# Performance work log

Measured on AMD Instinct MI355X. Metric: run time of the kernel, lower is better.

Reference implementation:

```python
import jax, jax.numpy as jnp
import numpy as np

N_NODES = 100000
N_EDGES = 1600000
IN_DIM = 128
OUT_DIM = 64


def setup_inputs() -> dict:
    key = jax.random.key(0)
    k1, k2, k3 = jax.random.split(key, 3)
    x = jax.random.normal(k1, (N_NODES, IN_DIM), dtype=jnp.float32)
    edge_index = jax.random.randint(k2, (2, N_EDGES), 0, N_NODES, dtype=jnp.int64)
    W = jax.random.normal(k3, (IN_DIM, OUT_DIM), dtype=jnp.float32) * (1.0 / np.sqrt(IN_DIM))
    b = jnp.zeros((OUT_DIM,), dtype=jnp.float32)
    return {"x": x, "edge_index": edge_index, "W": W, "b": b}


def reference(x, edge_index, W, b):
    row = edge_index[0]  # source nodes
    col = edge_index[1]  # target nodes (aggregation index)
    n = x.shape[0]

    # gcn_norm with add_self_loops=False: degree from edge weights (ones) at target
    ones = jnp.ones((edge_index.shape[1],), dtype=x.dtype)
    deg = jax.ops.segment_sum(ones, col, num_segments=n)  # [N]
    deg_inv_sqrt = jnp.where(deg > 0, jax.lax.rsqrt(jnp.maximum(deg, 1e-12)), 0.0)
    norm = deg_inv_sqrt[row] * deg_inv_sqrt[col]  # [E]

    # linear transform first (bias added after aggregation, as in PyG GCNConv)
    h = x @ W  # [N, OUT_DIM]

    # gather source features, scale by norm, scatter-add to targets
    msg = h[row] * norm[:, None]  # [E, OUT_DIM]
    out = jax.ops.segment_sum(msg, col, num_segments=n) + b  # [N, OUT_DIM]

    return jax.nn.relu(out)
```

## Files before the change

### kernel.cpp

```cpp
#include <hip/hip_runtime.h>
#include <hip/hip_bf16.h>

#define IN_DIM 128
#define OUT_DIM 64
#define FLOG 7
#define FNPB (1 << FLOG)
#define MAXFINE 1024
#define BB 512
#define BT 512
#define MAXE 8
#define NGRP 8
#define CAP_G 512
#define CAP (NGRP * CAP_G)
#define SPILL_MAX 65536

static inline size_t align_up(size_t v, size_t a) { return (v + a - 1) & ~(a - 1); }

__device__ __forceinline__ unsigned short f2bf(float f) {
    unsigned int x = __float_as_uint(f);
    unsigned int r = (x + 0x7fffu + ((x >> 16) & 1u)) >> 16;
    return (unsigned short)r;
}

typedef _Float16 half8 __attribute__((ext_vector_type(8)));
typedef float f32x4 __attribute__((ext_vector_type(4)));

__global__ void __launch_bounds__(BT, 4) k_build_mm(
    const int* __restrict__ row, const int* __restrict__ col,
    int* __restrict__ BinSize, unsigned int* __restrict__ EdgeBuf,
    uint2* __restrict__ spill, int* __restrict__ spillcur,
    const float* __restrict__ x, const float* __restrict__ W,
    unsigned short* __restrict__ h,
    int n_edges, int n_nodes, int nbf, int chunk, int mm_blocks) {
    if ((int)blockIdx.x < BB) {
        __shared__ int hist[MAXFINE];
        int t = threadIdx.x;
        int g = blockIdx.x & (NGRP - 1);
        int start = blockIdx.x * chunk;
        int end = min(n_edges, start + chunk);
        int n = end - start;

        for (int i = t; i < nbf; i += BT) hist[i] = 0;
        __syncthreads();

        int er[MAXE], ec[MAXE];
#pragma unroll
        for (int u = 0; u < MAXE; ++u) {
            int i = t + u * BT;
            ec[u] = -1;
            if (i < n) {
                er[u] = row[start + i];
                int c = col[start + i];
                ec[u] = c;
                atomicAdd(&hist[c >> FLOG], 1);
            }
        }
        __syncthreads();
        for (int i = t; i < nbf; i += BT) {
            int cv = hist[i];
            hist[i] = cv ? atomicAdd(&BinSize[g * nbf + i], cv) : 0;
        }
        __syncthreads();
#pragma unroll
        for (int u = 0; u < MAXE; ++u) {
            int c = ec[u];
            if (c >= 0) {
                int bin = c >> FLOG;
                int pos = atomicAdd(&hist[bin], 1);
                if (pos < CAP_G) {
                    EdgeBuf[(size_t)bin * CAP + g * CAP_G + pos] =
                        ((unsigned int)er[u] << FLOG) | (unsigned int)(c & (FNPB - 1));
                } else {
                    int sp = atomicAdd(spillcur, 1);
                    if (sp < SPILL_MAX)
                        spill[sp] = make_uint2((unsigned int)er[u], (unsigned int)c);
                }
            }
        }
    } else {
        const int lane = threadIdx.x & 63;
        const int m = lane & 15;
        const int q = lane >> 4;
        const int wv = threadIdx.x >> 6;
        const int wid0 = ((int)blockIdx.x - BB) * 8 + wv;
        const int nwaves = mm_blocks * 8;
        const int ntiles = (n_nodes + 15) >> 4;

        half8 bfrag[4][4];
#pragma unroll
        for (int kt = 0; kt < 4; ++kt) {
#pragma unroll
            for (int nt = 0; nt < 4; ++nt) {
                int k0 = kt * 32 + q * 8;
                int c = nt * 16 + m;
#pragma unroll
                for (int j = 0; j < 8; ++j)
                    bfrag[kt][nt][j] = (_Float16)W[(size_t)(k0 + j) * OUT_DIM + c];
            }
        }

        for (int wid = wid0; wid < ntiles; wid += nwaves) {
            const int nb = wid << 4;
            int arow = nb + m;
            if (arow >= n_nodes) arow = n_nodes - 1;
            const float* xr = x + (size_t)arow * IN_DIM;

            f32x4 acc[4];
#pragma unroll
            for (int nt = 0; nt < 4; ++nt) acc[nt] = (f32x4){0.f, 0.f, 0.f, 0.f};

#pragma unroll
            for (int kt = 0; kt < 4; ++kt) {
                const float4* xp = (const float4*)(xr + kt * 32 + q * 8);
                float4 lo = xp[0];
                float4 hi = xp[1];
                half8 afrag;
                afrag[0] = (_Float16)lo.x; afrag[1] = (_Float16)lo.y;
                afrag[2] = (_Float16)lo.z; afrag[3] = (_Float16)lo.w;
                afrag[4] = (_Float16)hi.x; afrag[5] = (_Float16)hi.y;
                afrag[6] = (_Float16)hi.z; afrag[7] = (_Float16)hi.w;
#pragma unroll
                for (int nt = 0; nt < 4; ++nt)
                    acc[nt] = __builtin_amdgcn_mfma_f32_16x16x32_f16(
                        afrag, bfrag[kt][nt], acc[nt], 0, 0, 0);
            }

#pragma unroll
            for (int r = 0; r < 4; ++r) {
                int node = nb + q * 4 + r;
                if (node < n_nodes) {
                    unsigned short* hp = h + (size_t)node * OUT_DIM + m;
#pragma unroll
                    for (int nt = 0; nt < 4; ++nt)
                        hp[nt * 16] = f2bf(acc[nt][r]);
                }
            }
        }
    }
}

__global__ void __launch_bounds__(256) kD_degree(
    const unsigned int* __restrict__ EdgeBuf, const int* __restrict__ BinSize,
    const uint2* __restrict__ spill, const int* __restrict__ spillcur,
    float* __restrict__ dis, int* __restrict__ cntg, int n_nodes, int nbf) {
    __shared__ int cnt[FNPB];
    int t = threadIdx.x;
    int b = blockIdx.x;
    if (t < FNPB) cnt[t] = 0;
    __syncthreads();
    for (int g = 0; g < NGRP; ++g) {
        int szg = min(BinSize[g * nbf + b], CAP_G);
        const unsigned int* sl = EdgeBuf + (size_t)b * CAP + g * CAP_G;
        for (int i = t; i < szg; i += 256)
            atomicAdd(&cnt[sl[i] & (FNPB - 1)], 1);
    }
    int sn = min(*spillcur, SPILL_MAX);
    for (int i = t; i < sn; i += 256) {
        uint2 e = spill[i];
        if ((int)(e.y >> FLOG) == b) atomicAdd(&cnt[e.y & (FNPB - 1)], 1);
    }
    __syncthreads();
    if (t < FNPB) {
        int d = cnt[t];
        cntg[(size_t)b * FNPB + t] = d;
        int node = (b << FLOG) + t;
        if (node < n_nodes)
            dis[node] = (d > 0) ? rsqrtf((float)d) : 0.0f;
    }
}

__global__ void __launch_bounds__(512) kF_sortagg(
    const unsigned int* __restrict__ EdgeBuf, const int* __restrict__ BinSize,
    const uint2* __restrict__ spill, const int* __restrict__ spillcur,
    const unsigned short* __restrict__ h, const float* __restrict__ dis,
    const int* __restrict__ cntg, const float* __restrict__ b,
    float* __restrict__ out, int* __restrict__ arena, int* __restrict__ arenacur,
    int n_nodes, int nbf) {
    __shared__ int cnt[FNPB];
    __shared__ int seg[FNPB];
    __shared__ int cursor[FNPB];
    __shared__ int sbuf[CAP];
    __shared__ int abase_sh;
    int t = threadIdx.x;
    int bk = blockIdx.x;
    int nb0 = bk << FLOG;
    int sn = min(*spillcur, SPILL_MAX);

    if (t < 64) {
        int2 cc = *(const int2*)(cntg + (size_t)bk * FNPB + 2 * t);
        int s = cc.x + cc.y;
#pragma unroll
        for (int off = 1; off < 64; off <<= 1) {
            int y = __shfl_up(s, off, 64);
            if (t >= off) s += y;
        }
        cnt[2 * t] = cc.x;
        cnt[2 * t + 1] = cc.y;
        seg[2 * t + 1] = s;
        seg[2 * t] = s - cc.y;
        cursor[2 * t] = s - cc.y - cc.x;
        cursor[2 * t + 1] = s - cc.y;
    }
    __syncthreads();

    int ne = seg[FNPB - 1];
    if (t == 0 && ne > CAP) abase_sh = atomicAdd(arenacur, ne);
    __syncthreads();

    const int lane = t & 63;
    const int wv = t >> 6;
    const int quarter = lane >> 4;
    const int qlane = lane & 15;
    float4 bias = ((const float4*)b)[qlane];

    if (ne <= CAP) {
        for (int g = 0; g < NGRP; ++g) {
            int szg = min(BinSize[g * nbf + bk], CAP_G);
            const unsigned int* sl = EdgeBuf + (size_t)bk * CAP + g * CAP_G;
            for (int i = t; i < szg; i += 512) {
                unsigned int v = sl[i];
                int p = atomicAdd(&cursor[v & (FNPB - 1)], 1);
                sbuf[p] = (int)(v >> FLOG);
            }
        }
        for (int i = t; i < sn; i += 512) {
            uint2 e = spill[i];
            if ((int)(e.y >> FLOG) == bk) {
                int p = atomicAdd(&cursor[e.y & (FNPB - 1)], 1);
                sbuf[p] = (int)e.x;
            }
        }
        __syncthreads();

        for (int nl = wv; nl < FNPB; nl += 8) {
            int node = nb0 + nl;
            if (node >= n_nodes) break;
            int e_ = seg[nl];
            int dcount = cnt[nl];
            int s_ = e_ - dcount;
            float a0 = 0.f, a1 = 0.f, a2 = 0.f, a3 = 0.f;
            for (int j0 = s_; j0 < e_; j0 += 16) {
                int i0 = j0 + quarter;
                int i1 = i0 + 4;
                int i2 = i0 + 8;
                int i3 = i0 + 12;
                int r0 = sbuf[i0 < e_ ? i0 : s_];
                int r1 = sbuf[i1 < e_ ? i1 : s_];
                int r2 = sbuf[i2 < e_ ? i2 : s_];
                int r3 = sbuf[i3 < e_ ? i3 : s_];
                float d0 = dis[r0];
                float d1 = dis[r1];
                float d2 = dis[r2];
                float d3 = dis[r3];
                uint2 v0 = make_uint2(0u, 0u), v1 = v0, v2 = v0, v3 = v0;
                if (i0 < e_)
                    v0 = *(const uint2*)(h + (size_t)r0 * OUT_DIM + qlane * 4);
                if (i1 < e_)
                    v1 = *(const uint2*)(h + (size_t)r1 * OUT_DIM + qlane * 4);
                if (i2 < e_)
                    v2 = *(const uint2*)(h + (size_t)r2 * OUT_DIM + qlane * 4);
                if (i3 < e_)
                    v3 = *(const uint2*)(h + (size_t)r3 * OUT_DIM + qlane * 4);
                a0 = fmaf(__uint_as_float(v0.x << 16), d0, a0);
                a1 = fmaf(__uint_as_float(v0.x & 0xFFFF0000u), d0, a1);
                a2 = fmaf(__uint_as_float(v0.y << 16), d0, a2);
                a3 = fmaf(__uint_as_float(v0.y & 0xFFFF0000u), d0, a3);
                a0 = fmaf(__uint_as_float(v1.x << 16), d1, a0);
                a1 = fmaf(__uint_as_float(v1.x & 0xFFFF0000u), d1, a1);
                a2 = fmaf(__uint_as_float(v1.y << 16), d1, a2);
                a3 = fmaf(__uint_as_float(v1.y & 0xFFFF0000u), d1, a3);
                a0 = fmaf(__uint_as_float(v2.x << 16), d2, a0);
                a1 = fmaf(__uint_as_float(v2.x & 0xFFFF0000u), d2, a1);
                a2 = fmaf(__uint_as_float(v2.y << 16), d2, a2);
                a3 = fmaf(__uint_as_float(v2.y & 0xFFFF0000u), d2, a3);
                a0 = fmaf(__uint_as_float(v3.x << 16), d3, a0);
                a1 = fmaf(__uint_as_float(v3.x & 0xFFFF0000u), d3, a1);
                a2 = fmaf(__uint_as_float(v3.y << 16), d3, a2);
                a3 = fmaf(__uint_as_float(v3.y & 0xFFFF0000u), d3, a3);
            }
            a0 += __shfl_xor(a0, 16, 64); a0 += __shfl_xor(a0, 32, 64);
            a1 += __shfl_xor(a1, 16, 64); a1 += __shfl_xor(a1, 32, 64);
            a2 += __shfl_xor(a2, 16, 64); a2 += __shfl_xor(a2, 32, 64);
            a3 += __shfl_xor(a3, 16, 64); a3 += __shfl_xor(a3, 32, 64);
            if (quarter == 0) {
                float dv = (dcount > 0) ? rsqrtf((float)dcount) : 0.0f;
                float4 o;
                o.x = fmaxf(fmaf(a0, dv, bias.x), 0.f);
                o.y = fmaxf(fmaf(a1, dv, bias.y), 0.f);
                o.z = fmaxf(fmaf(a2, dv, bias.z), 0.f);
                o.w = fmaxf(fmaf(a3, dv, bias.w), 0.f);
                ((float4*)(out + (size_t)node * OUT_DIM))[qlane] = o;
            }
        }
    } else {
        int abase = abase_sh;
        for (int g = 0; g < NGRP; ++g) {
            int szg = min(BinSize[g * nbf + bk], CAP_G);
            const unsigned int* sl = EdgeBuf + (size_t)bk * CAP + g * CAP_G;
            for (int i = t; i < szg; i += 512) {
                unsigned int v = sl[i];
                int p = atomicAdd(&cursor[v & (FNPB - 1)], 1);
                arena[abase + p] = (int)(v >> FLOG);
            }
        }
        for (int i = t; i < sn; i += 512) {
            uint2 e = spill[i];
            if ((int)(e.y >> FLOG) == bk) {
                int p = atomicAdd(&cursor[e.y & (FNPB - 1)], 1);
                arena[abase + p] = (int)e.x;
            }
        }
        __threadfence();
        __syncthreads();
        for (int nl = wv; nl < FNPB; nl += 8) {
            int node = nb0 + nl;
            if (node >= n_nodes) break;
            int e_ = seg[nl];
            int dcount = cnt[nl];
            int s_ = e_ - dcount;
            float a0 = 0.f, a1 = 0.f, a2 = 0.f, a3 = 0.f;
            for (int j0 = s_; j0 < e_; j0 += 8) {
                int iA = j0 + quarter;
                int iB = j0 + quarter + 4;
                int rA = arena[abase + (iA < e_ ? iA : s_)];
                int rB = arena[abase + (iB < e_ ? iB : s_)];
                float dA = dis[rA];
                float dB = dis[rB];
                uint2 vA = make_uint2(0u, 0u), vB = make_uint2(0u, 0u);
                if (iA < e_)
                    vA = *(const uint2*)(h + (size_t)rA * OUT_DIM + qlane * 4);
                if (iB < e_)
                    vB = *(const uint2*)(h + (size_t)rB * OUT_DIM + qlane * 4);
                a0 = fmaf(__uint_as_float(vA.x << 16), dA, a0);
                a1 = fmaf(__uint_as_float(vA.x & 0xFFFF0000u), dA, a1);
                a2 = fmaf(__uint_as_float(vA.y << 16), dA, a2);
                a3 = fmaf(__uint_as_float(vA.y & 0xFFFF0000u), dA, a3);
                a0 = fmaf(__uint_as_float(vB.x << 16), dB, a0);
                a1 = fmaf(__uint_as_float(vB.x & 0xFFFF0000u), dB, a1);
                a2 = fmaf(__uint_as_float(vB.y << 16), dB, a2);
                a3 = fmaf(__uint_as_float(vB.y & 0xFFFF0000u), dB, a3);
            }
            a0 += __shfl_xor(a0, 16, 64); a0 += __shfl_xor(a0, 32, 64);
            a1 += __shfl_xor(a1, 16, 64); a1 += __shfl_xor(a1, 32, 64);
            a2 += __shfl_xor(a2, 16, 64); a2 += __shfl_xor(a2, 32, 64);
            a3 += __shfl_xor(a3, 16, 64); a3 += __shfl_xor(a3, 32, 64);
            if (quarter == 0) {
                float dv = (dcount > 0) ? rsqrtf((float)dcount) : 0.0f;
                float4 o;
                o.x = fmaxf(fmaf(a0, dv, bias.x), 0.f);
                o.y = fmaxf(fmaf(a1, dv, bias.y), 0.f);
                o.z = fmaxf(fmaf(a2, dv, bias.z), 0.f);
                o.w = fmaxf(fmaf(a3, dv, bias.w), 0.f);
                ((float4*)(out + (size_t)node * OUT_DIM))[qlane] = o;
            }
        }
    }
}

#define MM_NODES 16
__global__ void __launch_bounds__(256) k_matmul_f32(
    const float* __restrict__ x, const float* __restrict__ W,
    const float* __restrict__ dis, float* __restrict__ h, int n_nodes) {
    __shared__ float xs[MM_NODES * IN_DIM];
    const int lane = threadIdx.x & 63;
    const int wv = threadIdx.x >> 6;
    float w[IN_DIM];
#pragma unroll
    for (int k = 0; k < IN_DIM; ++k) w[k] = W[k * OUT_DIM + lane];
    int nchunks = (n_nodes + MM_NODES - 1) / MM_NODES;
    for (int ch = blockIdx.x; ch < nchunks; ch += gridDim.x) {
        int base = ch * MM_NODES;
        int nrows = min(MM_NODES, n_nodes - base);
        __syncthreads();
        const float4* xg = (const float4*)(x + (size_t)base * IN_DIM);
        int nf4 = nrows * IN_DIM / 4;
        for (int i = threadIdx.x; i < nf4; i += 256) ((float4*)xs)[i] = xg[i];
        __syncthreads();
#pragma unroll
        for (int j = 0; j < 4; ++j) {
            int local = wv * 4 + j;
            int node = base + local;
            if (local < nrows) {
                const float4* xr = (const float4*)(xs + local * IN_DIM);
                float acc = 0.0f;
#pragma unroll
                for (int k4 = 0; k4 < IN_DIM / 4; ++k4) {
                    float4 xv = xr[k4];
                    acc = fmaf(xv.x, w[k4 * 4 + 0], acc);
                    acc = fmaf(xv.y, w[k4 * 4 + 1], acc);
                    acc = fmaf(xv.z, w[k4 * 4 + 2], acc);
                    acc = fmaf(xv.w, w[k4 * 4 + 3], acc);
                }
                h[(size_t)node * OUT_DIM + lane] = acc * dis[node];
            }
        }
    }
}

__global__ void k_degree_fb(const int* __restrict__ col, int* __restrict__ deg,
                            int n_edges) {
    int i = blockIdx.x * blockDim.x + threadIdx.x;
    int stride = gridDim.x * blockDim.x;
    for (; i < n_edges; i += stride) atomicAdd(&deg[col[i]], 1);
}

__global__ void k_rsqrt_fb(const int* __restrict__ deg, float* __restrict__ dis, int n) {
    int i = blockIdx.x * blockDim.x + threadIdx.x;
    if (i < n) {
        int d = deg[i];
        dis[i] = (d > 0) ? rsqrtf((float)d) : 0.0f;
    }
}

__global__ void __launch_bounds__(256) k_scatter_fb(
    const int* __restrict__ row, const int* __restrict__ col,
    const float* __restrict__ dis, const float* __restrict__ h,
    float* __restrict__ out, int n_edges) {
    const int lane = threadIdx.x & 63;
    int e = (blockIdx.x * blockDim.x + threadIdx.x) >> 6;
    int nw = (gridDim.x * blockDim.x) >> 6;
    for (; e < n_edges; e += nw) {
        int r = row[e];
        int c = col[e];
        float v = h[(size_t)r * OUT_DIM + lane] * dis[c];
        atomicAdd(&out[(size_t)c * OUT_DIM + lane], v);
    }
}

__global__ void k_bias_relu_fb(float* __restrict__ out, const float* __restrict__ b,
                               int total) {
    int i = blockIdx.x * blockDim.x + threadIdx.x;
    int stride = gridDim.x * blockDim.x;
    for (; i < total; i += stride) {
        float v = out[i] + b[i & (OUT_DIM - 1)];
        out[i] = fmaxf(v, 0.0f);
    }
}

extern "C" void kernel_launch(void* const* d_in, const int* in_sizes, int n_in,
                              void* d_out, int out_size, void* d_ws, size_t ws_size,
                              hipStream_t stream) {
    const float* x = (const float*)d_in[0];
    const int* ei = (const int*)d_in[1];
    const float* W = (const float*)d_in[2];
    const float* b = (const float*)d_in[3];
    float* out = (float*)d_out;

    const int n_nodes = in_sizes[0] / IN_DIM;
    const int n_edges = in_sizes[1] / 2;
    const int* row = ei;
    const int* col = ei + n_edges;

    const int nbf = (n_nodes + FNPB - 1) >> FLOG;
    const int chunk = (n_edges + BB - 1) / BB;

    char* wsb = (char*)d_ws;
    size_t off = 0;
    int* BinSize = (int*)(wsb + off);    off += (size_t)(nbf * NGRP + 8) * 4;
    int* spillcur = BinSize + nbf * NGRP;
    int* arenacur = BinSize + nbf * NGRP + 1;
    const size_t zero_bytes = off;
    off = align_up(off, 256);
    unsigned int* EdgeBuf = (unsigned int*)(wsb + off);
                                         off += align_up((size_t)nbf * CAP * 4, 256);
    uint2* spill = (uint2*)(wsb + off);  off += align_up((size_t)SPILL_MAX * 8, 256);
    int* arena = (int*)(wsb + off);      off += align_up((size_t)n_edges * 4, 256);
    float* dis = (float*)(wsb + off);    off += align_up((size_t)n_nodes * 4, 256);
    int* cntg = (int*)(wsb + off);       off += align_up((size_t)nbf * FNPB * 4, 256);
    unsigned short* h = (unsigned short*)(wsb + off);
                                         off += (size_t)n_nodes * OUT_DIM * 2;
    const size_t needed = off;

    const bool ok = (ws_size >= needed) && (nbf <= MAXFINE) &&
                    (chunk <= MAXE * BT) && (n_nodes <= (1 << 24));

    if (ok) {
        const int ntiles = (n_nodes + 15) >> 4;
        int mm_blocks = (ntiles + 15) / 16;
        if (mm_blocks < 1) mm_blocks = 1;
        hipMemsetAsync(BinSize, 0, zero_bytes, stream);
        k_build_mm<<<BB + mm_blocks, BT, 0, stream>>>(
            row, col, BinSize, EdgeBuf, spill, spillcur,
            x, W, h, n_edges, n_nodes, nbf, chunk, mm_blocks);
        kD_degree<<<nbf, 256, 0, stream>>>(EdgeBuf, BinSize, spill, spillcur,
                                           dis, cntg, n_nodes, nbf);
        kF_sortagg<<<nbf, 512, 0, stream>>>(EdgeBuf, BinSize, spill, spillcur,
                                            h, dis, cntg, b, out, arena, arenacur,
                                            n_nodes, nbf);
    } else {
        char* p = (char*)d_ws;
        int* deg_f = (int*)p;
        float* dis_f = (float*)(p + align_up((size_t)n_nodes * 4, 256));
        float* h_f = (float*)(p + 2 * align_up((size_t)n_nodes * 4, 256));
        hipMemsetAsync(deg_f, 0, (size_t)n_nodes * 4, stream);
        hipMemsetAsync(out, 0, (size_t)out_size * 4, stream);
        k_degree_fb<<<1024, 256, 0, stream>>>(col, deg_f, n_edges);
        k_rsqrt_fb<<<(n_nodes + 255) / 256, 256, 0, stream>>>(deg_f, dis_f, n_nodes);
        k_matmul_f32<<<1024, 256, 0, stream>>>(x, W, dis_f, h_f, n_nodes);
        k_scatter_fb<<<2048, 256, 0, stream>>>(row, col, dis_f, h_f, out, n_edges);
        k_bias_relu_fb<<<2048, 256, 0, stream>>>(out, b, n_nodes * OUT_DIM);
    }
}
```

Before: 174.5 us.

## Split sort-aggregate blocks into two half-bin blocks of 256 threads

The sort-and-aggregate kernel now launches two blocks per fine bin, each handling 64 of the 128 target nodes with 256 threads and a smaller shared sort buffer. This doubles the grid (about 782 to 1564 blocks) and shrinks LDS per block, aiming to raise occupancy and spread work across more CUs. In exchange, each block re-reads the whole bin's edge list and the spill list and discards about half the entries. The smaller shared buffer may also send more bins to the global arena path.

New measurement: 172.2 us, median of 2. Within noise of the previous version (-1.3%).

```diff
diff --git a/kernel.cpp b/kernel.cpp
--- a/kernel.cpp
+++ b/kernel.cpp
@@ -13,6 +13,9 @@
 #define CAP_G 512
 #define CAP (NGRP * CAP_G)
 #define SPILL_MAX 65536
+#define KFT 256
+#define HALF 64
+#define SBUF_CAP 2048
 
 static inline size_t align_up(size_t v, size_t a) { return (v + a - 1) & ~(a - 1); }
 
@@ -169,42 +172,41 @@
     }
 }
 
-__global__ void __launch_bounds__(512) kF_sortagg(
+__global__ void __launch_bounds__(KFT) kF_sortagg(
     const unsigned int* __restrict__ EdgeBuf, const int* __restrict__ BinSize,
     const uint2* __restrict__ spill, const int* __restrict__ spillcur,
     const unsigned short* __restrict__ h, const float* __restrict__ dis,
     const int* __restrict__ cntg, const float* __restrict__ b,
     float* __restrict__ out, int* __restrict__ arena, int* __restrict__ arenacur,
     int n_nodes, int nbf) {
-    __shared__ int cnt[FNPB];
-    __shared__ int seg[FNPB];
-    __shared__ int cursor[FNPB];
-    __shared__ int sbuf[CAP];
+    __shared__ int cnt[HALF];
+    __shared__ int seg[HALF];
+    __shared__ int cursor[HALF];
+    __shared__ int sbuf[SBUF_CAP];
     __shared__ int abase_sh;
     int t = threadIdx.x;
-    int bk = blockIdx.x;
-    int nb0 = bk << FLOG;
+    int bk = blockIdx.x >> 1;
+    int halfid = blockIdx.x & 1;
+    int lo = halfid * HALF;
+    int nb0 = (bk << FLOG) + lo;
     int sn = min(*spillcur, SPILL_MAX);
 
     if (t < 64) {
-        int2 cc = *(const int2*)(cntg + (size_t)bk * FNPB + 2 * t);
-        int s = cc.x + cc.y;
+        int c = cntg[(size_t)bk * FNPB + lo + t];
+        int s = c;
 #pragma unroll
         for (int off = 1; off < 64; off <<= 1) {
             int y = __shfl_up(s, off, 64);
             if (t >= off) s += y;
         }
-        cnt[2 * t] = cc.x;
-        cnt[2 * t + 1] = cc.y;
-        seg[2 * t + 1] = s;
-        seg[2 * t] = s - cc.y;
-        cursor[2 * t] = s - cc.y - cc.x;
-        cursor[2 * t + 1] = s - cc.y;
+        cnt[t] = c;
+        seg[t] = s;
+        cursor[t] = s - c;
     }
     __syncthreads();
 
-    int ne = seg[FNPB - 1];
-    if (t == 0 && ne > CAP) abase_sh = atomicAdd(arenacur, ne);
+    int ne = seg[HALF - 1];
+    if (t == 0 && ne > SBUF_CAP) abase_sh = atomicAdd(arenacur, ne);
     __syncthreads();
 
     const int lane = t & 63;
@@ -213,26 +215,32 @@
     const int qlane = lane & 15;
     float4 bias = ((const float4*)b)[qlane];
 
-    if (ne <= CAP) {
+    if (ne <= SBUF_CAP) {
         for (int g = 0; g < NGRP; ++g) {
             int szg = min(BinSize[g * nbf + bk], CAP_G);
             const unsigned int* sl = EdgeBuf + (size_t)bk * CAP + g * CAP_G;
-            for (int i = t; i < szg; i += 512) {
+            for (int i = t; i < szg; i += KFT) {
                 unsigned int v = sl[i];
-                int p = atomicAdd(&cursor[v & (FNPB - 1)], 1);
-                sbuf[p] = (int)(v >> FLOG);
-            }
-        }
-        for (int i = t; i < sn; i += 512) {
+                int nlocal = (int)(v & (FNPB - 1)) - lo;
+                if ((unsigned)nlocal < HALF) {
+                    int p = atomicAdd(&cursor[nlocal], 1);
+                    sbuf[p] = (int)(v >> FLOG);
+                }
+            }
+        }
+        for (int i = t; i < sn; i += KFT) {
             uint2 e = spill[i];
             if ((int)(e.y >> FLOG) == bk) {
-                int p = atomicAdd(&cursor[e.y & (FNPB - 1)], 1);
-                sbuf[p] = (int)e.x;
-            }
-        }
-        __syncthreads();
-
-        for (int nl = wv; nl < FNPB; nl += 8) {
+                int nlocal = (int)(e.y & (FNPB - 1)) - lo;
+                if ((unsigned)nlocal < HALF) {
+                    int p = atomicAdd(&cursor[nlocal], 1);
+                    sbuf[p] = (int)e.x;
+                }
+            }
+        }
+        __syncthreads();
+
+        for (int nl = wv; nl < HALF; nl += 4) {
             int node = nb0 + nl;
             if (node >= n_nodes) break;
             int e_ = seg[nl];
@@ -297,22 +305,28 @@
         for (int g = 0; g < NGRP; ++g) {
             int szg = min(BinSize[g * nbf + bk], CAP_G);
             const unsigned int* sl = EdgeBuf + (size_t)bk * CAP + g * CAP_G;
-            for (int i = t; i < szg; i += 512) {
+            for (int i = t; i < szg; i += KFT) {
                 unsigned int v = sl[i];
-                int p = atomicAdd(&cursor[v & (FNPB - 1)], 1);
-                arena[abase + p] = (int)(v >> FLOG);
-            }
-        }
-        for (int i = t; i < sn; i += 512) {
+                int nlocal = (int)(v & (FNPB - 1)) - lo;
+                if ((unsigned)nlocal < HALF) {
+                    int p = atomicAdd(&cursor[nlocal], 1);
+                    arena[abase + p] = (int)(v >> FLOG);
+                }
+            }
+        }
+        for (int i = t; i < sn; i += KFT) {
             uint2 e = spill[i];
             if ((int)(e.y >> FLOG) == bk) {
-                int p = atomicAdd(&cursor[e.y & (FNPB - 1)], 1);
-                arena[abase + p] = (int)e.x;
+                int nlocal = (int)(e.y & (FNPB - 1)) - lo;
+                if ((unsigned)nlocal < HALF) {
+                    int p = atomicAdd(&cursor[nlocal], 1);
+                    arena[abase + p] = (int)e.x;
+                }
             }
         }
         __threadfence();
         __syncthreads();
-        for (int nl = wv; nl < FNPB; nl += 8) {
+        for (int nl = wv; nl < HALF; nl += 4) {
             int node = nb0 + nl;
             if (node >= n_nodes) break;
             int e_ = seg[nl];
@@ -484,9 +498,9 @@
             x, W, h, n_edges, n_nodes, nbf, chunk, mm_blocks);
         kD_degree<<<nbf, 256, 0, stream>>>(EdgeBuf, BinSize, spill, spillcur,
                                            dis, cntg, n_nodes, nbf);
-        kF_sortagg<<<nbf, 512, 0, stream>>>(EdgeBuf, BinSize, spill, spillcur,
-                                            h, dis, cntg, b, out, arena, arenacur,
-                                            n_nodes, nbf);
+        kF_sortagg<<<2 * nbf, KFT, 0, stream>>>(EdgeBuf, BinSize, spill, spillcur,
+                                                h, dis, cntg, b, out, arena,
+                                                arenacur, n_nodes, nbf);
     } else {
         char* p = (char*)d_ws;
         int* deg_f = (int*)p;
```
